# Kernel tuning notes

Hardware: AMD Instinct MI355X
Metric: run time of the kernel (lower is better)

Reference implementation:

```python
import jax, jax.numpy as jnp
import numpy as np

B, Ci, Pi, Co, Po, K = 8, 8, 16, 16, 16, 3
H = W = 64


def setup_inputs() -> dict:
    key = jax.random.key(0)
    k1, k2 = jax.random.split(key)
    x = jax.random.normal(k1, (B, Ci, Pi, H, W), dtype=jnp.float32)
    # Conv2d weight, torch OIHW layout: [Co*Po, Pi, K, K]
    conv_w = jax.random.normal(k2, (Co * Po, Pi, K, K), dtype=jnp.float32) * 0.05
    biases = jnp.full((1, 1, Co, Po, 1, 1), 0.1, dtype=jnp.float32)
    return {"x": x, "conv_w": conv_w, "biases": biases, "routings": 3}


def squash(sj):
    # sj: [B,1,Co,Po,Ho,Wo]; squash along pose dim (axis=3)
    sjnorm = jnp.linalg.norm(sj, axis=3, keepdims=True)
    sjnorm2 = sjnorm ** 2
    return sjnorm2 * sj / ((1.0 + sjnorm2) * sjnorm)


def reference(x, conv_w, biases, routings):
    b, ci, pi, h, w = x.shape
    # shared conv applied per input capsule channel
    xr = x.reshape(b * ci, pi, h, w)
    y = jax.lax.conv_general_dilated(
        xr, conv_w, window_strides=(1, 1), padding=((1, 1), (1, 1)),
        dimension_numbers=("NCHW", "OIHW", "NCHW"))
    ho, wo = y.shape[2], y.shape[3]
    votes = y.reshape(b, ci, Co, Po, ho, wo)  # [B,Ci,Co,Po,Ho,Wo]

    bij = jnp.zeros((b, ci, Co, 1, ho, wo), dtype=votes.dtype)
    vj = None
    for t in range(routings):
        cij = jax.nn.softmax(bij, axis=2)               # over output capsules
        sj = jnp.sum(cij * votes, axis=1, keepdims=True) + biases
        vj = squash(sj)                                 # [B,1,Co,Po,Ho,Wo]
        if t < routings - 1:
            bij = bij + jnp.sum(votes * vj, axis=3, keepdims=True)
    return vj.squeeze(1)  # [B,Co,Po,Ho,Wo]
```

## Files before the change

kernel.cpp:

```cpp
#include <hip/hip_runtime.h>


namespace {
constexpr int CI = 8, PIn = 16, H = 64, Wd = 64;
constexpr int TP = 8;
constexpr int NQ = 8;
constexpr int CIW = 244;
constexpr int KT = 5;
constexpr int BBO = 1088;
}

typedef __fp16 h2  __attribute__((ext_vector_type(2)));
typedef __fp16 f16x8 __attribute__((ext_vector_type(8)));
typedef float  f32x4 __attribute__((ext_vector_type(4)));

__device__ __forceinline__ h2 pkh(float a, float b) {
#if __has_builtin(__builtin_amdgcn_cvt_pkrtz)
    return __builtin_amdgcn_cvt_pkrtz(a, b);
#else
    h2 r; r[0] = (__fp16)a; r[1] = (__fp16)b; return r;
#endif
}

template<int CTRL>
__device__ __forceinline__ float dppmovf(float x) {
    return __builtin_bit_cast(float,
        __builtin_amdgcn_mov_dpp(__builtin_bit_cast(int, x), CTRL, 0xf, 0xf, true));
}
template<int CTRL>
__device__ __forceinline__ float dppadd(float x) { return x + dppmovf<CTRL>(x); }

__device__ __forceinline__ float rsum16(float x) {
    x += dppmovf<0x121>(x); x += dppmovf<0x122>(x);
    x += dppmovf<0x124>(x); x += dppmovf<0x128>(x);
    return x;
}
__device__ __forceinline__ float rmax16(float x) {
    x = fmaxf(x, dppmovf<0x121>(x)); x = fmaxf(x, dppmovf<0x122>(x));
    x = fmaxf(x, dppmovf<0x124>(x)); x = fmaxf(x, dppmovf<0x128>(x));
    return x;
}
__device__ __forceinline__ float swz_xor16(float x) {
    return __builtin_bit_cast(float,
        __builtin_amdgcn_ds_swizzle(__builtin_bit_cast(int, x), 0x401F));
}

__global__ __launch_bounds__(256)
void prep_wfrag(const float* __restrict__ w, __fp16* __restrict__ wf) {
    const int gid = blockIdx.x * 256 + threadIdx.x;
    if (gid >= KT * 16 * 64) return;
    const int l = gid & 63, m = (gid >> 6) & 15, kt = gid >> 10;
    const int oc = m * 16 + (l & 15);
    h2* dp = reinterpret_cast<h2*>(wf + (size_t)gid * 8);
    #pragma unroll
    for (int jw = 0; jw < 4; ++jw) {
        const int k0 = kt * 32 + (l >> 4) * 8 + jw * 2;
        float f0 = 0.f, f1 = 0.f;
        if (k0 < 144)     f0 = w[oc * 144 + (k0 & 15) * 9 + (k0 >> 4)];
        if (k0 + 1 < 144) f1 = w[oc * 144 + ((k0 + 1) & 15) * 9 + ((k0 + 1) >> 4)];
        dp[jw] = pkh(f0, f1);
    }
}

__global__ __launch_bounds__(256, 5)
void convcaps_mfma(const float* __restrict__ x,
                   const __fp16* __restrict__ wf,
                   const float* __restrict__ biases,
                   const int* __restrict__ routings_p,
                   float* __restrict__ out)
{
    const int t    = threadIdx.x;
    const int lane = t & 63;
    const int wv   = t >> 6;
    const int g    = lane >> 4;
    const int nl   = lane & 15;
    const int n    = wv * 16 + nl;
    const int p_   = n >> 3, ci_ = n & 7;
    const int gh   = g >> 1;
    const int ql   = (g & 1) * 4;

    const int blk  = (blockIdx.x & 7) * 512 + (blockIdx.x >> 3);
    const int wseg = blk & 7;
    const int ho   = (blk >> 3) & 63;
    const int b    = blk >> 9;
    const int wo0  = wseg * TP;
    const int routings = routings_p[0];

    __shared__ float  shu[2816];
    alignas(16) __shared__ float ccl[64 * 20];
    __shared__ float  bl[256];
    h2*    xs    = reinterpret_cast<h2*>(shu);
    float* bb    = shu;
    float* vjlds = shu;

    if (t < 192) {
        const int ci  = t / 24;
        const int rem = t - ci * 24;
        const int r   = rem >> 3, q = rem & 7;
        const int hy  = ho - 1 + r;
        const bool rowok = (hy >= 0) && (hy < H);
        const float* row0 = x + (((size_t)(b * CI + ci) * PIn + 2 * q) * H + hy) * Wd;
        const float* row1 = row0 + H * Wd;
        float4 m0a = {0,0,0,0}, m1a = {0,0,0,0}, m0b = {0,0,0,0}, m1b = {0,0,0,0};
        float  e0a = 0.f, e0b = 0.f, e9a = 0.f, e9b = 0.f;
        if (rowok) {
            m0a = *reinterpret_cast<const float4*>(row0 + wo0);
            m1a = *reinterpret_cast<const float4*>(row0 + wo0 + 4);
            m0b = *reinterpret_cast<const float4*>(row1 + wo0);
            m1b = *reinterpret_cast<const float4*>(row1 + wo0 + 4);
            if (wo0 > 0)       { e0a = row0[wo0 - 1]; e0b = row1[wo0 - 1]; }
            if (wo0 + 8 < Wd)  { e9a = row0[wo0 + 8]; e9b = row1[wo0 + 8]; }
        }
        h2* xr = &xs[ci * CIW + (r * 10) * 8 + q];
        xr[0 * 8] = pkh(e0a, e0b);
        xr[1 * 8] = pkh(m0a.x, m0b.x);
        xr[2 * 8] = pkh(m0a.y, m0b.y);
        xr[3 * 8] = pkh(m0a.z, m0b.z);
        xr[4 * 8] = pkh(m0a.w, m0b.w);
        xr[5 * 8] = pkh(m1a.x, m1b.x);
        xr[6 * 8] = pkh(m1a.y, m1b.y);
        xr[7 * 8] = pkh(m1a.z, m1b.z);
        xr[8 * 8] = pkh(m1a.w, m1b.w);
        xr[9 * 8] = pkh(e9a, e9b);
    }
    bl[t] = biases[t];
    __syncthreads();

    f32x4 acc[16];
    #pragma unroll
    for (int m = 0; m < 16; ++m) acc[m] = f32x4{0.f, 0.f, 0.f, 0.f};

    const f16x8* ap = reinterpret_cast<const f16x8*>(wf);
    #pragma unroll
    for (int kt = 0; kt < KT; ++kt) {
        f16x8 bfrag;
        const int k0 = kt * 32 + g * 8;
        if (k0 < 144) {
            const int r9 = 2 * kt + gh;
            const int kh = (r9 * 11) >> 5;
            const int kw = r9 - 3 * kh;
            bfrag = *reinterpret_cast<const f16x8*>(
                &xs[ci_ * CIW + (kh * 10 + p_ + kw) * 8 + ql]);
        } else {
            bfrag = f16x8{(__fp16)0.f, (__fp16)0.f, (__fp16)0.f, (__fp16)0.f,
                          (__fp16)0.f, (__fp16)0.f, (__fp16)0.f, (__fp16)0.f};
        }
        #pragma unroll
        for (int m = 0; m < 16; ++m) {
            const f16x8 afrag = ap[(kt * 16 + m) * 64 + lane];
            acc[m] = __builtin_amdgcn_mfma_f32_16x16x32_f16(afrag, bfrag, acc[m], 0, 0, 0);
        }
    }
    __syncthreads();

    for (int it = 0; it < routings; ++it) {
        const bool first  = (it == 0);
        const bool lastit = (it + 1 >= routings);

        f32x4 cw4[4];
        if (!first) {
            #pragma unroll
            for (int k2 = 0; k2 < 4; ++k2) {
                const int i   = t + 256 * k2;
                const int idx = (i >> 4) * 17 + (i & 15);
                const float bv = bb[idx] + bb[BBO + idx];
                const float mx = rmax16(bv);
                const float e  = __expf(bv - mx);
                const float sd = rsum16(e);
                ccl[(i >> 4) * 20 + (i & 15)] = e * __builtin_amdgcn_rcpf(sd);
            }
            __syncthreads();
            const f32x4* cwp = reinterpret_cast<const f32x4*>(&ccl[n * 20]);
            cw4[0] = cwp[0]; cw4[1] = cwp[1]; cw4[2] = cwp[2]; cw4[3] = cwp[3];
        }

        #pragma unroll
        for (int m = 0; m < 16; ++m) {
            const float cw = first ? 0.0625f : cw4[m >> 2][m & 3];
            float s0 = cw * acc[m][0], s1 = cw * acc[m][1];
            float s2 = cw * acc[m][2], s3 = cw * acc[m][3];
            s0 = dppadd<0xB1>(s0);  s1 = dppadd<0xB1>(s1);
            s2 = dppadd<0xB1>(s2);  s3 = dppadd<0xB1>(s3);
            s0 = dppadd<0x4E>(s0);  s1 = dppadd<0x4E>(s1);
            s2 = dppadd<0x4E>(s2);  s3 = dppadd<0x4E>(s3);
            s0 = dppadd<0x141>(s0); s1 = dppadd<0x141>(s1);
            s2 = dppadd<0x141>(s2); s3 = dppadd<0x141>(s3);
            const f32x4 b4 = *reinterpret_cast<const f32x4*>(&bl[m * 16 + g * 4]);
            s0 += b4[0]; s1 += b4[1]; s2 += b4[2]; s3 += b4[3];
            float q2 = s0 * s0 + s1 * s1 + s2 * s2 + s3 * s3;
            q2 += swz_xor16(q2);
            q2 += __shfl_xor(q2, 32, 64);
            const float sc = __fsqrt_rn(q2) * __builtin_amdgcn_rcpf(1.f + q2);
            const float v0 = s0 * sc, v1 = s1 * sc, v2 = s2 * sc, v3 = s3 * sc;
            if (!lastit) {
                float uu = acc[m][0] * v0 + acc[m][1] * v1
                         + acc[m][2] * v2 + acc[m][3] * v3;
                uu += swz_xor16(uu);
                if ((g & 1) == 0) {
                    const int idx = (g << 9) + (g << 5) + n * 17 + m;
                    if (first) bb[idx] = uu;
                    else       bb[idx] += uu;
                }
            } else if (ci_ == 0) {
                const int oc = m * 16 + g * 4;
                vjlds[(oc + 0) * 11 + p_] = v0;
                vjlds[(oc + 1) * 11 + p_] = v1;
                vjlds[(oc + 2) * 11 + p_] = v2;
                vjlds[(oc + 3) * 11 + p_] = v3;
            }
        }
        __syncthreads();
    }

    float o[8];
    #pragma unroll
    for (int j = 0; j < 8; ++j) o[j] = vjlds[t * 11 + j];
    float* op = out + ((size_t)(b * 256 + t)) * (H * Wd) + ho * Wd + wo0;
    *reinterpret_cast<float4*>(op)     = make_float4(o[0], o[1], o[2], o[3]);
    *reinterpret_cast<float4*>(op + 4) = make_float4(o[4], o[5], o[6], o[7]);
}

extern "C" void kernel_launch(void* const* d_in, const int* in_sizes, int n_in,
                              void* d_out, int out_size, void* d_ws, size_t ws_size,
                              hipStream_t stream) {
    const float* x       = (const float*)d_in[0];
    const float* w       = (const float*)d_in[1];
    const float* biases  = (const float*)d_in[2];
    const int*   routing = (const int*)d_in[3];
    float* out = (float*)d_out;
    __fp16* wf = (__fp16*)d_ws;

    hipLaunchKernelGGL(prep_wfrag, dim3(20), dim3(256), 0, stream, w, wf);
    hipLaunchKernelGGL(convcaps_mfma, dim3(8 * 64 * (64 / TP)), dim3(256), 0, stream,
                       x, wf, biases, routing, out);
}
```

Before: 127.6 us.

## Retile MFMA work so each wave owns 4 M-tiles by 4 N-tiles

Each wave used to compute all 16 output-channel tiles for a single 16-column N tile, which meant loading every A (weight) fragment from global memory in every wave. Now each wave handles 4 M tiles across all 4 N tiles. Each A fragment is loaded once and reused across 4 B fragments read from LDS, which cuts global weight traffic per block by a factor of four. The routing epilogue index math and the bias and coupling-weight loads are remapped to match, and the bias is hoisted into registers. The cost is more LDS reads of the B operand per wave.

```diff
diff --git a/kernel.cpp b/kernel.cpp
--- a/kernel.cpp
+++ b/kernel.cpp
@@ -74,8 +74,8 @@
     const int wv   = t >> 6;
     const int g    = lane >> 4;
     const int nl   = lane & 15;
-    const int n    = wv * 16 + nl;
-    const int p_   = n >> 3, ci_ = n & 7;
+    const int ci_  = nl & 7;
+    const int pb   = nl >> 3;
     const int gh   = g >> 1;
     const int ql   = (g & 1) * 4;
 
@@ -88,7 +88,7 @@
 
     __shared__ float  shu[2816];
     alignas(16) __shared__ float ccl[64 * 20];
-    __shared__ float  bl[256];
+    alignas(16) __shared__ float bl[256];
     h2*    xs    = reinterpret_cast<h2*>(shu);
     float* bb    = shu;
     float* vjlds = shu;
@@ -126,31 +126,45 @@
     bl[t] = biases[t];
     __syncthreads();
 
-    f32x4 acc[16];
-    #pragma unroll
-    for (int m = 0; m < 16; ++m) acc[m] = f32x4{0.f, 0.f, 0.f, 0.f};
+    f32x4 acc[4][4];
+    #pragma unroll
+    for (int mi = 0; mi < 4; ++mi)
+        #pragma unroll
+        for (int nt = 0; nt < 4; ++nt) acc[mi][nt] = f32x4{0.f, 0.f, 0.f, 0.f};
 
     const f16x8* ap = reinterpret_cast<const f16x8*>(wf);
     #pragma unroll
     for (int kt = 0; kt < KT; ++kt) {
-        f16x8 bfrag;
+        f16x8 bfr[4];
         const int k0 = kt * 32 + g * 8;
         if (k0 < 144) {
             const int r9 = 2 * kt + gh;
             const int kh = (r9 * 11) >> 5;
             const int kw = r9 - 3 * kh;
-            bfrag = *reinterpret_cast<const f16x8*>(
-                &xs[ci_ * CIW + (kh * 10 + p_ + kw) * 8 + ql]);
+            const int base = ci_ * CIW + (kh * 10 + pb + kw) * 8 + ql;
+            #pragma unroll
+            for (int nt = 0; nt < 4; ++nt)
+                bfr[nt] = *reinterpret_cast<const f16x8*>(&xs[base + nt * 16]);
         } else {
-            bfrag = f16x8{(__fp16)0.f, (__fp16)0.f, (__fp16)0.f, (__fp16)0.f,
-                          (__fp16)0.f, (__fp16)0.f, (__fp16)0.f, (__fp16)0.f};
+            #pragma unroll
+            for (int nt = 0; nt < 4; ++nt)
+                bfr[nt] = f16x8{(__fp16)0.f, (__fp16)0.f, (__fp16)0.f, (__fp16)0.f,
+                                (__fp16)0.f, (__fp16)0.f, (__fp16)0.f, (__fp16)0.f};
         }
         #pragma unroll
-        for (int m = 0; m < 16; ++m) {
-            const f16x8 afrag = ap[(kt * 16 + m) * 64 + lane];
-            acc[m] = __builtin_amdgcn_mfma_f32_16x16x32_f16(afrag, bfrag, acc[m], 0, 0, 0);
-        }
-    }
+        for (int mi = 0; mi < 4; ++mi) {
+            const f16x8 afrag = ap[(kt * 16 + wv * 4 + mi) * 64 + lane];
+            #pragma unroll
+            for (int nt = 0; nt < 4; ++nt)
+                acc[mi][nt] = __builtin_amdgcn_mfma_f32_16x16x32_f16(
+                                  afrag, bfr[nt], acc[mi][nt], 0, 0, 0);
+        }
+    }
+
+    f32x4 bias4[4];
+    #pragma unroll
+    for (int mi = 0; mi < 4; ++mi)
+        bias4[mi] = *reinterpret_cast<const f32x4*>(&bl[(wv * 4 + mi) * 16 + g * 4]);
     __syncthreads();
 
     for (int it = 0; it < routings; ++it) {
@@ -170,43 +184,50 @@
                 ccl[(i >> 4) * 20 + (i & 15)] = e * __builtin_amdgcn_rcpf(sd);
             }
             __syncthreads();
-            const f32x4* cwp = reinterpret_cast<const f32x4*>(&ccl[n * 20]);
-            cw4[0] = cwp[0]; cw4[1] = cwp[1]; cw4[2] = cwp[2]; cw4[3] = cwp[3];
+            #pragma unroll
+            for (int nt = 0; nt < 4; ++nt)
+                cw4[nt] = *reinterpret_cast<const f32x4*>(
+                              &ccl[(nt * 16 + nl) * 20 + wv * 4]);
         }
 
         #pragma unroll
-        for (int m = 0; m < 16; ++m) {
-            const float cw = first ? 0.0625f : cw4[m >> 2][m & 3];
-            float s0 = cw * acc[m][0], s1 = cw * acc[m][1];
-            float s2 = cw * acc[m][2], s3 = cw * acc[m][3];
-            s0 = dppadd<0xB1>(s0);  s1 = dppadd<0xB1>(s1);
-            s2 = dppadd<0xB1>(s2);  s3 = dppadd<0xB1>(s3);
-            s0 = dppadd<0x4E>(s0);  s1 = dppadd<0x4E>(s1);
-            s2 = dppadd<0x4E>(s2);  s3 = dppadd<0x4E>(s3);
-            s0 = dppadd<0x141>(s0); s1 = dppadd<0x141>(s1);
-            s2 = dppadd<0x141>(s2); s3 = dppadd<0x141>(s3);
-            const f32x4 b4 = *reinterpret_cast<const f32x4*>(&bl[m * 16 + g * 4]);
-            s0 += b4[0]; s1 += b4[1]; s2 += b4[2]; s3 += b4[3];
-            float q2 = s0 * s0 + s1 * s1 + s2 * s2 + s3 * s3;
-            q2 += swz_xor16(q2);
-            q2 += __shfl_xor(q2, 32, 64);
-            const float sc = __fsqrt_rn(q2) * __builtin_amdgcn_rcpf(1.f + q2);
-            const float v0 = s0 * sc, v1 = s1 * sc, v2 = s2 * sc, v3 = s3 * sc;
-            if (!lastit) {
-                float uu = acc[m][0] * v0 + acc[m][1] * v1
-                         + acc[m][2] * v2 + acc[m][3] * v3;
-                uu += swz_xor16(uu);
-                if ((g & 1) == 0) {
-                    const int idx = (g << 9) + (g << 5) + n * 17 + m;
-                    if (first) bb[idx] = uu;
-                    else       bb[idx] += uu;
+        for (int mi = 0; mi < 4; ++mi) {
+            #pragma unroll
+            for (int nt = 0; nt < 4; ++nt) {
+                const float cw = first ? 0.0625f : cw4[nt][mi];
+                float s0 = cw * acc[mi][nt][0], s1 = cw * acc[mi][nt][1];
+                float s2 = cw * acc[mi][nt][2], s3 = cw * acc[mi][nt][3];
+                s0 = dppadd<0xB1>(s0);  s1 = dppadd<0xB1>(s1);
+                s2 = dppadd<0xB1>(s2);  s3 = dppadd<0xB1>(s3);
+                s0 = dppadd<0x4E>(s0);  s1 = dppadd<0x4E>(s1);
+                s2 = dppadd<0x4E>(s2);  s3 = dppadd<0x4E>(s3);
+                s0 = dppadd<0x141>(s0); s1 = dppadd<0x141>(s1);
+                s2 = dppadd<0x141>(s2); s3 = dppadd<0x141>(s3);
+                s0 += bias4[mi][0]; s1 += bias4[mi][1];
+                s2 += bias4[mi][2]; s3 += bias4[mi][3];
+                float q2 = s0 * s0 + s1 * s1 + s2 * s2 + s3 * s3;
+                q2 += swz_xor16(q2);
+                q2 += __shfl_xor(q2, 32, 64);
+                const float sc = __fsqrt_rn(q2) * __builtin_amdgcn_rcpf(1.f + q2);
+                const float v0 = s0 * sc, v1 = s1 * sc, v2 = s2 * sc, v3 = s3 * sc;
+                if (!lastit) {
+                    float uu = acc[mi][nt][0] * v0 + acc[mi][nt][1] * v1
+                             + acc[mi][nt][2] * v2 + acc[mi][nt][3] * v3;
+                    uu += swz_xor16(uu);
+                    if ((g & 1) == 0) {
+                        const int idx = (g << 9) + (g << 5)
+                                      + (nt * 16 + nl) * 17 + wv * 4 + mi;
+                        if (first) bb[idx] = uu;
+                        else       bb[idx] += uu;
+                    }
+                } else if (ci_ == 0) {
+                    const int oc = (wv * 4 + mi) * 16 + g * 4;
+                    const int p  = nt * 2 + pb;
+                    vjlds[(oc + 0) * 11 + p] = v0;
+                    vjlds[(oc + 1) * 11 + p] = v1;
+                    vjlds[(oc + 2) * 11 + p] = v2;
+                    vjlds[(oc + 3) * 11 + p] = v3;
                 }
-            } else if (ci_ == 0) {
-                const int oc = m * 16 + g * 4;
-                vjlds[(oc + 0) * 11 + p_] = v0;
-                vjlds[(oc + 1) * 11 + p_] = v1;
-                vjlds[(oc + 2) * 11 + p_] = v2;
-                vjlds[(oc + 3) * 11 + p_] = v3;
             }
         }
         __syncthreads();
```

Measured after the change: 163.6 us. 28.2% more time.
